# Optimization experiments

Measured on AMD Instinct MI355X. Metric: run time of the kernel, lower is better.

The kernel has to match this reference:

```python
import jax, jax.numpy as jnp
import numpy as np

N_GROUPS = 32
EPS = 1e-5


def group_norm(x, gamma, beta):
    b, c, h, w = x.shape
    xg = x.reshape(b, N_GROUPS, c // N_GROUPS, h, w)
    mean = xg.mean(axis=(2, 3, 4), keepdims=True)
    var = xg.var(axis=(2, 3, 4), keepdims=True)
    xn = ((xg - mean) * jax.lax.rsqrt(var + EPS)).reshape(b, c, h, w)
    return xn * gamma[None, :, None, None] + beta[None, :, None, None]


def conv1x1(x, W, b):
    # x: [b,c,h,w], W: [out,in], b: [out]
    return jnp.einsum('bchw,oc->bohw', x, W) + b[None, :, None, None]


def setup_inputs() -> dict:
    key = jax.random.key(0)
    ks = jax.random.split(key, 6)
    B, C, H, W = 8, 256, 64, 64
    s = 1.0 / np.sqrt(C)
    return {
        'x': jax.random.normal(ks[0], (B, C, H, W), dtype=jnp.float32),
        'norm_gamma': jnp.ones((C,), jnp.float32),
        'norm_beta': jnp.zeros((C,), jnp.float32),
        'Wq': jax.random.normal(ks[1], (C, C), jnp.float32) * s,
        'bq': jnp.zeros((C,), jnp.float32),
        'Wk': jax.random.normal(ks[2], (C, C), jnp.float32) * s,
        'bk': jnp.zeros((C,), jnp.float32),
        'Wv': jax.random.normal(ks[3], (C, C), jnp.float32) * s,
        'bv': jnp.zeros((C,), jnp.float32),
        'Wo': jax.random.normal(ks[4], (C, C), jnp.float32) * s,
        'bo': jnp.zeros((C,), jnp.float32),
    }


def reference(x, norm_gamma, norm_beta, Wq, bq, Wk, bk, Wv, bv, Wo, bo):
    b, c, h, w = x.shape
    hn = group_norm(x, norm_gamma, norm_beta)
    q = conv1x1(hn, Wq, bq).reshape(b, c, h * w)  # [b,c,hw]
    k = conv1x1(hn, Wk, bk).reshape(b, c, h * w)
    v = conv1x1(hn, Wv, bv).reshape(b, c, h * w)
    # scores[b,i,j] = sum_c q[b,c,i] * k[b,c,j]; scale is int(c)*-0.5
    # (faithful to the source, which multiplies by -0.5*c, NOT c**-0.5)
    scores = jnp.einsum('bci,bcj->bij', q, k) * (c * -0.5)
    attn = jax.nn.softmax(scores, axis=2)  # softmax over j (keys)
    # h_[b,c,i] = sum_j v[b,c,j] * attn[b,i,j]
    h_ = jnp.einsum('bcj,bij->bci', v, attn).reshape(b, c, h, w)
    # source applies self.out to the ORIGINAL input x and adds attention output
    return h_ + conv1x1(x, Wo, bo)
```

## Files before the change

### kernel.cpp

```cpp
#include <hip/hip_runtime.h>
#include <hip/hip_bf16.h>


typedef __attribute__((ext_vector_type(8))) short bf16x8;
typedef __attribute__((ext_vector_type(4))) short s16x4;
typedef __attribute__((ext_vector_type(8))) short s16x8;
typedef __attribute__((ext_vector_type(4))) float f32x4;

#define MFMA16(a, b, c) __builtin_amdgcn_mfma_f32_16x16x32_bf16((a), (b), (c), 0, 0, 0)

#define SCALE_Q (-184.66496523378734f)

__device__ __forceinline__ short f2bf(float f) {
  unsigned int u = __builtin_bit_cast(unsigned int, f);
  u = (u + 0x7FFFu + ((u >> 16) & 1u)) >> 16;
  return (short)(unsigned short)u;
}
__device__ __forceinline__ short t2bf(float f) {
  return (short)(__builtin_bit_cast(unsigned int, f) >> 16);
}
__device__ __forceinline__ float bf2f(short h) {
  unsigned int u = ((unsigned int)(unsigned short)h) << 16;
  return __builtin_bit_cast(float, u);
}
__device__ __forceinline__ void async16(void* lds, const void* g) {
  __builtin_amdgcn_global_load_lds(
      (const __attribute__((address_space(1))) unsigned int*)g,
      (__attribute__((address_space(3))) unsigned int*)lds, 16, 0, 0);
}
__device__ __forceinline__ void lgkm_barrier() {
  asm volatile("s_waitcnt lgkmcnt(0)" ::: "memory");
  __builtin_amdgcn_s_barrier();
  __builtin_amdgcn_sched_barrier(0);
}

__global__ void wsplit_k(const float* __restrict__ Wq, const float* __restrict__ Wk,
                         const float* __restrict__ Wv, const float* __restrict__ Wo,
                         short* __restrict__ whi, short* __restrict__ wlo) {
  int idx = blockIdx.x * 256 + threadIdx.x;
  int m = idx >> 16;
  int e = idx & 65535;
  const float* W = (m == 0) ? Wq : (m == 1) ? Wk : (m == 2) ? Wv : Wo;
  float v = W[e];
  short h = f2bf(v);
  whi[idx] = h;
  wlo[idx] = f2bf(v - bf2f(h));
}

__global__ __launch_bounds__(256) void gn_fused_k(
    const float* __restrict__ x, const float* __restrict__ gamma,
    const float* __restrict__ beta, short* __restrict__ hn_hi,
    short* __restrict__ hn_lo) {
  int b = blockIdx.x, g = blockIdx.y, tid = threadIdx.x;
  const float* p = x + ((size_t)(b * 32 + g)) * 32768;
  float s = 0.f, sq = 0.f;
  for (int it = 0; it < 32; ++it) {
    f32x4 v = *(const f32x4*)(p + (size_t)(it * 256 + tid) * 4);
    s += v[0] + v[1] + v[2] + v[3];
    sq += v[0] * v[0] + v[1] * v[1] + v[2] * v[2] + v[3] * v[3];
  }
#pragma unroll
  for (int off = 1; off < 64; off <<= 1) {
    s += __shfl_xor(s, off);
    sq += __shfl_xor(sq, off);
  }
  __shared__ float ls[4], lq[4];
  if ((tid & 63) == 0) { ls[tid >> 6] = s; lq[tid >> 6] = sq; }
  __syncthreads();
  float S = ls[0] + ls[1] + ls[2] + ls[3];
  float Q = lq[0] + lq[1] + lq[2] + lq[3];
  float mean = S * (1.f / 32768.f);
  float rstd = rsqrtf(Q * (1.f / 32768.f) - mean * mean + 1e-5f);
  int c0 = g * 8;
  float ga[8], be[8];
#pragma unroll
  for (int cc = 0; cc < 8; ++cc) {
    ga[cc] = gamma[c0 + cc] * rstd;
    be[cc] = beta[c0 + cc] - mean * ga[cc];
  }
  for (int it = 0; it < 16; ++it) {
    int i = it * 256 + tid;
    s16x8 hv, lv;
#pragma unroll
    for (int cc = 0; cc < 8; ++cc) {
      float xv = p[(size_t)cc * 4096 + i];
      float h = xv * ga[cc] + be[cc];
      short hh = f2bf(h);
      hv[cc] = hh;
      lv[cc] = f2bf(h - bf2f(hh));
    }
    size_t ro = ((size_t)(b * 4096 + i)) * 256 + c0;
    *(s16x8*)(hn_hi + ro) = hv;
    *(s16x8*)(hn_lo + ro) = lv;
  }
}

__global__ __launch_bounds__(256) void proj_qk_k(
    const short* __restrict__ hn_hi, const short* __restrict__ hn_lo,
    const short* __restrict__ whi, const short* __restrict__ wlo,
    const float* __restrict__ bq, const float* __restrict__ bk,
    short* __restrict__ q_hi, short* __restrict__ q_lo,
    short* __restrict__ k_hi, short* __restrict__ k_lo) {
  int tid = threadIdx.x, w = tid >> 6, lane = tid & 63, l4 = lane & 15, g = lane >> 4;
  int iblk = blockIdx.x, y = blockIdx.y, b = blockIdx.z;
  const short* wh = whi + y * 65536;
  const short* wl = wlo + y * 65536;
  const float* bias = y ? bk : bq;
  short* ohi = (y ? k_hi : q_hi) + (size_t)b * 1048576;
  short* olo = (y ? k_lo : q_lo) + (size_t)b * 1048576;
  float scale = y ? 1.0f : SCALE_Q;
  int arow = iblk * 64 + w * 16 + l4;
  const short* ha = hn_hi + ((size_t)(b * 4096 + arow)) * 256 + g * 8;
  const short* la = hn_lo + ((size_t)(b * 4096 + arow)) * 256 + g * 8;
  f32x4 acc[16];
#pragma unroll
  for (int i = 0; i < 16; ++i) acc[i] = (f32x4){0.f, 0.f, 0.f, 0.f};
  for (int ks = 0; ks < 8; ++ks) {
    bf16x8 ah = *(const bf16x8*)(ha + ks * 32);
    bf16x8 al = *(const bf16x8*)(la + ks * 32);
#pragma unroll
    for (int ct = 0; ct < 16; ++ct) {
      bf16x8 bh = *(const bf16x8*)(wh + (ct * 16 + l4) * 256 + ks * 32 + g * 8);
      bf16x8 bl = *(const bf16x8*)(wl + (ct * 16 + l4) * 256 + ks * 32 + g * 8);
      acc[ct] = MFMA16(ah, bh, acc[ct]);
      acc[ct] = MFMA16(al, bh, acc[ct]);
      acc[ct] = MFMA16(ah, bl, acc[ct]);
    }
  }
  int orow = iblk * 64 + w * 16 + g * 4;
#pragma unroll
  for (int ct = 0; ct < 16; ++ct) {
    int c = ct * 16 + l4;
    float bsv = bias[c];
#pragma unroll
    for (int r = 0; r < 4; ++r) {
      float val = (acc[ct][r] + bsv) * scale;
      short h = f2bf(val);
      short lo = f2bf(val - bf2f(h));
      size_t off = ((size_t)(orow + r)) * 256 + c;
      ohi[off] = h;
      olo[off] = lo;
    }
  }
}

__global__ __launch_bounds__(256) void proj_v_k(
    const short* __restrict__ hn_hi, const short* __restrict__ wv_hi,
    const float* __restrict__ bv, short* __restrict__ vout) {
  int tid = threadIdx.x, w = tid >> 6, lane = tid & 63, l4 = lane & 15, g = lane >> 4;
  int jblk = blockIdx.x, cblk = blockIdx.y, b = blockIdx.z;
  int crow = cblk * 64 + w * 16 + l4;
  const short* ap = wv_hi + (size_t)crow * 256 + g * 8;
  f32x4 acc[4];
#pragma unroll
  for (int i = 0; i < 4; ++i) acc[i] = (f32x4){0.f, 0.f, 0.f, 0.f};
  for (int ks = 0; ks < 8; ++ks) {
    bf16x8 a = *(const bf16x8*)(ap + ks * 32);
#pragma unroll
    for (int jt = 0; jt < 4; ++jt) {
      bf16x8 bb = *(const bf16x8*)(hn_hi +
          ((size_t)(b * 4096 + jblk * 64 + jt * 16 + l4)) * 256 + ks * 32 + g * 8);
      acc[jt] = MFMA16(a, bb, acc[jt]);
    }
  }
#pragma unroll
  for (int jt = 0; jt < 4; ++jt) {
#pragma unroll
    for (int r = 0; r < 4; ++r) {
      int c = cblk * 64 + w * 16 + g * 4 + r;
      int j = jblk * 64 + jt * 16 + l4;
      float val = acc[jt][r] + bv[c];
      vout[((size_t)(b * 256 + c)) * 4096 + j] = f2bf(val);
    }
  }
}

__global__ __launch_bounds__(256, 2) void flash3c_k(
    const short* __restrict__ qhi, const short* __restrict__ qlo,
    const short* __restrict__ khi, const short* __restrict__ klo,
    const short* __restrict__ vv, const float* __restrict__ x,
    const short* __restrict__ wo_hi, const float* __restrict__ bo,
    float* __restrict__ out) {
  __shared__ short k_hi_s[2][8192];
  __shared__ short k_lo_s[2][8192];
  __shared__ short p_s[2048];
  __shared__ __attribute__((aligned(16))) float albuf[64];
  __shared__ __attribute__((aligned(16))) float flagbuf[4];
  __shared__ __attribute__((aligned(16))) float lsmbuf[64];

  int tid = threadIdx.x, w = tid >> 6, lane = tid & 63, l4 = lane & 15, g = lane >> 4;
  int b = blockIdx.x, i0 = blockIdx.y * 64;
  size_t boff = (size_t)b * 1048576;
  const short* qh_p = qhi + boff;
  const short* ql_p = qlo + boff;
  const char* kh_g = (const char*)(khi + boff);
  const char* kl_g = (const char*)(klo + boff);
  const short* v_p = vv + boff;

  int qrow = i0 + w * 16 + l4;
  bf16x8 qh[8], ql[8];
#pragma unroll
  for (int ks = 0; ks < 8; ++ks) {
    qh[ks] = *(const bf16x8*)(qh_p + (size_t)qrow * 256 + ks * 32 + g * 8);
    ql[ks] = *(const bf16x8*)(ql_p + (size_t)qrow * 256 + ks * 32 + g * 8);
  }

  f32x4 oac[4][4];
#pragma unroll
  for (int it = 0; it < 4; ++it)
#pragma unroll
    for (int ct = 0; ct < 4; ++ct) oac[it][ct] = (f32x4){0.f, 0.f, 0.f, 0.f};
  float m_cur = -1e30f, lsum = 0.f;

  int ksrc[4];
#pragma unroll
  for (int it = 0; it < 4; ++it) {
    int U = it * 256 + tid;
    int jrow = ((U >> 6) & 1) * 16 + (U & 15);
    ksrc[it] = jrow * 512 + (U >> 7) * 64 + ((U >> 4) & 3) * 16;
  }
  int koff = g * 256 + l4 * 16;
  int pwb = w * 1024 + (g >> 1) * 256 + l4 * 16 + (g & 1) * 8;
  char* khs = (char*)k_hi_s;
  char* kls = (char*)k_lo_s;
  char* ps = (char*)p_s;
  int cbase = w * 64;
  bf16x8 vreg[4];

#pragma unroll
  for (int it = 0; it < 4; ++it) {
    int ldst = w * 1024 + it * 4096;
    async16(khs + ldst, kh_g + ksrc[it]);
    async16(kls + ldst, kl_g + ksrc[it]);
  }

  for (int js = 0; js < 128; ++js) {
    int cur = (js & 1) * 16384;
    __syncthreads();
#pragma unroll
    for (int ct = 0; ct < 4; ++ct)
      vreg[ct] = *(const bf16x8*)(v_p + (size_t)(cbase + ct * 16 + l4) * 4096 +
                                  js * 32 + g * 8);
    if (js < 127) {
      int kgo = (js + 1) * 16384;
      int nxt = ((js + 1) & 1) * 16384;
#pragma unroll
      for (int it = 0; it < 4; ++it) {
        int ldst = nxt + w * 1024 + it * 4096;
        async16(khs + ldst, kh_g + kgo + ksrc[it]);
        async16(kls + ldst, kl_g + kgo + ksrc[it]);
      }
    }

    f32x4 st0 = (f32x4){0.f, 0.f, 0.f, 0.f};
    f32x4 st1 = (f32x4){0.f, 0.f, 0.f, 0.f};
    __builtin_amdgcn_s_setprio(1);
#pragma unroll
    for (int ks = 0; ks < 8; ++ks) {
      bf16x8 kh0 = *(const bf16x8*)(khs + cur + ks * 2048 + koff);
      bf16x8 kh1 = *(const bf16x8*)(khs + cur + ks * 2048 + 1024 + koff);
      bf16x8 kl0 = *(const bf16x8*)(kls + cur + ks * 2048 + koff);
      bf16x8 kl1 = *(const bf16x8*)(kls + cur + ks * 2048 + 1024 + koff);
      st0 = MFMA16(kh0, qh[ks], st0);
      st1 = MFMA16(kh1, qh[ks], st1);
      st0 = MFMA16(kl0, qh[ks], st0);
      st1 = MFMA16(kl1, qh[ks], st1);
      st0 = MFMA16(kh0, ql[ks], st0);
      st1 = MFMA16(kh1, ql[ks], st1);
    }
    __builtin_amdgcn_s_setprio(0);

    float pmax = fmaxf(fmaxf(fmaxf(st0[0], st0[1]), fmaxf(st0[2], st0[3])),
                       fmaxf(fmaxf(st1[0], st1[1]), fmaxf(st1[2], st1[3])));
    pmax = fmaxf(pmax, __shfl_xor(pmax, 16));
    pmax = fmaxf(pmax, __shfl_xor(pmax, 32));
    float alpha = 1.0f;
    bool upd = !__all(pmax <= m_cur + 11.0f);
    if (upd) {
      float m_new = fmaxf(m_cur, pmax);
      alpha = exp2f(m_cur - m_new);
      lsum *= alpha;
      m_cur = m_new;
    }
    f32x4 e0, e1;
#pragma unroll
    for (int r = 0; r < 4; ++r) {
      e0[r] = exp2f(st0[r] - m_cur);
      e1[r] = exp2f(st1[r] - m_cur);
    }
    float lps = e0[0] + e0[1] + e0[2] + e0[3] + e1[0] + e1[1] + e1[2] + e1[3];
    lps += __shfl_xor(lps, 16);
    lps += __shfl_xor(lps, 32);
    lsum += lps;

    s16x4 pw0 = {t2bf(e0[0]), t2bf(e0[1]), t2bf(e0[2]), t2bf(e0[3])};
    s16x4 pw1 = {t2bf(e1[0]), t2bf(e1[1]), t2bf(e1[2]), t2bf(e1[3])};
    *(s16x4*)(ps + pwb) = pw0;
    *(s16x4*)(ps + pwb + 512) = pw1;
    if (lane < 16) albuf[w * 16 + lane] = alpha;
    if (lane == 0) flagbuf[w] = upd ? 1.f : 0.f;

    lgkm_barrier();

    f32x4 fl = *(const f32x4*)(&flagbuf[0]);
    if (fl[0] + fl[1] + fl[2] + fl[3] > 0.f) {
#pragma unroll
      for (int it = 0; it < 4; ++it) {
        f32x4 av = *(const f32x4*)(&albuf[it * 16 + g * 4]);
#pragma unroll
        for (int ct = 0; ct < 4; ++ct)
#pragma unroll
          for (int r = 0; r < 4; ++r) oac[it][ct][r] *= av[r];
      }
    }
    __builtin_amdgcn_s_setprio(1);
#pragma unroll
    for (int it = 0; it < 4; ++it) {
      bf16x8 pf = *(const bf16x8*)(ps + it * 1024 + koff);
#pragma unroll
      for (int ct = 0; ct < 4; ++ct) oac[it][ct] = MFMA16(pf, vreg[ct], oac[it][ct]);
    }
    __builtin_amdgcn_s_setprio(0);
  }

  if (lane < 16) lsmbuf[w * 16 + lane] = lsum;
  __syncthreads();
#pragma unroll
  for (int it = 0; it < 4; ++it) {
    f32x4 lv = *(const f32x4*)(&lsmbuf[it * 16 + g * 4]);
    f32x4 iv = {1.f / lv[0], 1.f / lv[1], 1.f / lv[2], 1.f / lv[3]};
#pragma unroll
    for (int ct = 0; ct < 4; ++ct)
#pragma unroll
      for (int r = 0; r < 4; ++r) oac[it][ct][r] *= iv[r];
  }
  const float* xb = x + (size_t)b * 1048576;
  for (int ks = 0; ks < 8; ++ks) {
    bf16x8 af[4], bfr[4];
#pragma unroll
    for (int it = 0; it < 4; ++it) {
#pragma unroll
      for (int e = 0; e < 8; ++e) {
        float xv = xb[(size_t)(ks * 32 + g * 8 + e) * 4096 + i0 + it * 16 + l4];
        af[it][e] = t2bf(xv);
      }
    }
#pragma unroll
    for (int ct = 0; ct < 4; ++ct)
      bfr[ct] = *(const bf16x8*)(wo_hi + (cbase + ct * 16 + l4) * 256 + ks * 32 + g * 8);
#pragma unroll
    for (int it = 0; it < 4; ++it)
#pragma unroll
      for (int ct = 0; ct < 4; ++ct) oac[it][ct] = MFMA16(af[it], bfr[ct], oac[it][ct]);
  }
  float* ob = out + (size_t)b * 1048576;
#pragma unroll
  for (int ct = 0; ct < 4; ++ct) {
    float bov = bo[cbase + ct * 16 + l4];
#pragma unroll
    for (int it = 0; it < 4; ++it) {
      float* ad = ob + (size_t)(cbase + ct * 16 + l4) * 4096 + i0 + it * 16 + g * 4;
      f32x4 res;
#pragma unroll
      for (int r = 0; r < 4; ++r) res[r] = oac[it][ct][r] + bov;
      *(f32x4*)ad = res;
    }
  }
}

extern "C" void kernel_launch(void* const* d_in, const int* in_sizes, int n_in,
                              void* d_out, int out_size, void* d_ws, size_t ws_size,
                              hipStream_t stream) {
  (void)in_sizes; (void)n_in; (void)out_size; (void)ws_size;
  const float* x = (const float*)d_in[0];
  const float* gamma = (const float*)d_in[1];
  const float* beta = (const float*)d_in[2];
  const float* Wq = (const float*)d_in[3];
  const float* bq = (const float*)d_in[4];
  const float* Wk = (const float*)d_in[5];
  const float* bk = (const float*)d_in[6];
  const float* Wv = (const float*)d_in[7];
  const float* bv = (const float*)d_in[8];
  const float* Wo = (const float*)d_in[9];
  const float* bo = (const float*)d_in[10];
  float* out = (float*)d_out;
  char* ws = (char*)d_ws;

  const size_t MB16 = 16777216;
  short* whi = (short*)(ws + 4096);
  short* wlo = (short*)(ws + 4096 + 524288);
  char* base = ws + 4096 + 2 * 524288;
  short* hnhi = (short*)(base);
  short* hnlo = (short*)(base + MB16);
  short* qhi = (short*)(base + 2 * MB16);
  short* qlo = (short*)(base + 3 * MB16);
  short* khi = (short*)(base + 4 * MB16);
  short* klo = (short*)(base + 5 * MB16);
  short* vvp = (short*)(base + 6 * MB16);

  wsplit_k<<<dim3(1024), dim3(256), 0, stream>>>(Wq, Wk, Wv, Wo, whi, wlo);
  gn_fused_k<<<dim3(8, 32), dim3(256), 0, stream>>>(x, gamma, beta, hnhi, hnlo);
  proj_qk_k<<<dim3(64, 2, 8), dim3(256), 0, stream>>>(hnhi, hnlo, whi, wlo, bq, bk,
                                                      qhi, qlo, khi, klo);
  proj_v_k<<<dim3(64, 4, 8), dim3(256), 0, stream>>>(hnhi, whi + 2 * 65536, bv, vvp);
  flash3c_k<<<dim3(8, 64), dim3(256), 0, stream>>>(qhi, qlo, khi, klo, vvp, x,
                                                   whi + 3 * 65536, bo, out);
}
```

Baseline: 565.8 us.

## Keep softmax probabilities in registers and give each wave all output channels

The PV stage changes from each wave owning 64 output channels for all 64 query rows to each wave owning its own 16 query rows across all 256 channels. The probability tile can then be handed to the MFMA operand through lane shuffles instead of an LDS round trip. This removes the per-iteration LDS writes, the second block barrier, and the alpha/flag exchange buffers, and makes the rescale wave-local. In exchange every wave now loads the full V slab (16 vector loads per iteration, replicated across 4 waves) and holds 16 V registers, which raises global/L2 traffic and register pressure.

```diff
diff --git a/kernel.cpp b/kernel.cpp
--- a/kernel.cpp
+++ b/kernel.cpp
@@ -3,9 +3,9 @@
 
 
 typedef __attribute__((ext_vector_type(8))) short bf16x8;
-typedef __attribute__((ext_vector_type(4))) short s16x4;
 typedef __attribute__((ext_vector_type(8))) short s16x8;
 typedef __attribute__((ext_vector_type(4))) float f32x4;
+typedef __attribute__((ext_vector_type(4))) unsigned u32x4;
 
 #define MFMA16(a, b, c) __builtin_amdgcn_mfma_f32_16x16x32_bf16((a), (b), (c), 0, 0, 0)
 
@@ -19,6 +19,10 @@
 __device__ __forceinline__ short t2bf(float f) {
   return (short)(__builtin_bit_cast(unsigned int, f) >> 16);
 }
+__device__ __forceinline__ unsigned pk2bf(float a, float b) {
+  return (__builtin_bit_cast(unsigned int, b) & 0xFFFF0000u) |
+         (__builtin_bit_cast(unsigned int, a) >> 16);
+}
 __device__ __forceinline__ float bf2f(short h) {
   unsigned int u = ((unsigned int)(unsigned short)h) << 16;
   return __builtin_bit_cast(float, u);
@@ -27,11 +31,6 @@
   __builtin_amdgcn_global_load_lds(
       (const __attribute__((address_space(1))) unsigned int*)g,
       (__attribute__((address_space(3))) unsigned int*)lds, 16, 0, 0);
-}
-__device__ __forceinline__ void lgkm_barrier() {
-  asm volatile("s_waitcnt lgkmcnt(0)" ::: "memory");
-  __builtin_amdgcn_s_barrier();
-  __builtin_amdgcn_sched_barrier(0);
 }
 
 __global__ void wsplit_k(const float* __restrict__ Wq, const float* __restrict__ Wk,
@@ -175,7 +174,7 @@
   }
 }
 
-__global__ __launch_bounds__(256, 2) void flash3c_k(
+__global__ __launch_bounds__(256, 2) void flash6_k(
     const short* __restrict__ qhi, const short* __restrict__ qlo,
     const short* __restrict__ khi, const short* __restrict__ klo,
     const short* __restrict__ vv, const float* __restrict__ x,
@@ -183,10 +182,6 @@
     float* __restrict__ out) {
   __shared__ short k_hi_s[2][8192];
   __shared__ short k_lo_s[2][8192];
-  __shared__ short p_s[2048];
-  __shared__ __attribute__((aligned(16))) float albuf[64];
-  __shared__ __attribute__((aligned(16))) float flagbuf[4];
-  __shared__ __attribute__((aligned(16))) float lsmbuf[64];
 
   int tid = threadIdx.x, w = tid >> 6, lane = tid & 63, l4 = lane & 15, g = lane >> 4;
   int b = blockIdx.x, i0 = blockIdx.y * 64;
@@ -205,11 +200,9 @@
     ql[ks] = *(const bf16x8*)(ql_p + (size_t)qrow * 256 + ks * 32 + g * 8);
   }
 
-  f32x4 oac[4][4];
-#pragma unroll
-  for (int it = 0; it < 4; ++it)
-#pragma unroll
-    for (int ct = 0; ct < 4; ++ct) oac[it][ct] = (f32x4){0.f, 0.f, 0.f, 0.f};
+  f32x4 oac[16];
+#pragma unroll
+  for (int ct = 0; ct < 16; ++ct) oac[ct] = (f32x4){0.f, 0.f, 0.f, 0.f};
   float m_cur = -1e30f, lsum = 0.f;
 
   int ksrc[4];
@@ -220,12 +213,9 @@
     ksrc[it] = jrow * 512 + (U >> 7) * 64 + ((U >> 4) & 3) * 16;
   }
   int koff = g * 256 + l4 * 16;
-  int pwb = w * 1024 + (g >> 1) * 256 + l4 * 16 + (g & 1) * 8;
   char* khs = (char*)k_hi_s;
   char* kls = (char*)k_lo_s;
-  char* ps = (char*)p_s;
-  int cbase = w * 64;
-  bf16x8 vreg[4];
+  bf16x8 vreg[16];
 
 #pragma unroll
   for (int it = 0; it < 4; ++it) {
@@ -234,13 +224,13 @@
     async16(kls + ldst, kl_g + ksrc[it]);
   }
 
+  int srcE = ((g & 1) << 5) + l4;
+  int srcO = srcE + 16;
+  bool gLo = (g < 2);
+
   for (int js = 0; js < 128; ++js) {
     int cur = (js & 1) * 16384;
     __syncthreads();
-#pragma unroll
-    for (int ct = 0; ct < 4; ++ct)
-      vreg[ct] = *(const bf16x8*)(v_p + (size_t)(cbase + ct * 16 + l4) * 4096 +
-                                  js * 32 + g * 8);
     if (js < 127) {
       int kgo = (js + 1) * 16384;
       int nxt = ((js + 1) & 1) * 16384;
@@ -251,6 +241,10 @@
         async16(kls + ldst, kl_g + kgo + ksrc[it]);
       }
     }
+#pragma unroll
+    for (int ct = 0; ct < 16; ++ct)
+      vreg[ct] = *(const bf16x8*)(v_p + (size_t)(ct * 16 + l4) * 4096 +
+                                  js * 32 + g * 8);
 
     f32x4 st0 = (f32x4){0.f, 0.f, 0.f, 0.f};
     f32x4 st1 = (f32x4){0.f, 0.f, 0.f, 0.f};
@@ -274,13 +268,18 @@
                        fmaxf(fmaxf(st1[0], st1[1]), fmaxf(st1[2], st1[3])));
     pmax = fmaxf(pmax, __shfl_xor(pmax, 16));
     pmax = fmaxf(pmax, __shfl_xor(pmax, 32));
-    float alpha = 1.0f;
-    bool upd = !__all(pmax <= m_cur + 11.0f);
-    if (upd) {
+    if (!__all(pmax <= m_cur + 11.0f)) {
       float m_new = fmaxf(m_cur, pmax);
-      alpha = exp2f(m_cur - m_new);
+      float alpha = exp2f(m_cur - m_new);
       lsum *= alpha;
       m_cur = m_new;
+      f32x4 av;
+#pragma unroll
+      for (int r = 0; r < 4; ++r) av[r] = __shfl(alpha, g * 4 + r);
+#pragma unroll
+      for (int ct = 0; ct < 16; ++ct)
+#pragma unroll
+        for (int r = 0; r < 4; ++r) oac[ct][r] *= av[r];
     }
     f32x4 e0, e1;
 #pragma unroll
@@ -293,78 +292,53 @@
     lps += __shfl_xor(lps, 32);
     lsum += lps;
 
-    s16x4 pw0 = {t2bf(e0[0]), t2bf(e0[1]), t2bf(e0[2]), t2bf(e0[3])};
-    s16x4 pw1 = {t2bf(e1[0]), t2bf(e1[1]), t2bf(e1[2]), t2bf(e1[3])};
-    *(s16x4*)(ps + pwb) = pw0;
-    *(s16x4*)(ps + pwb + 512) = pw1;
-    if (lane < 16) albuf[w * 16 + lane] = alpha;
-    if (lane == 0) flagbuf[w] = upd ? 1.f : 0.f;
-
-    lgkm_barrier();
-
-    f32x4 fl = *(const f32x4*)(&flagbuf[0]);
-    if (fl[0] + fl[1] + fl[2] + fl[3] > 0.f) {
-#pragma unroll
-      for (int it = 0; it < 4; ++it) {
-        f32x4 av = *(const f32x4*)(&albuf[it * 16 + g * 4]);
-#pragma unroll
-        for (int ct = 0; ct < 4; ++ct)
-#pragma unroll
-          for (int r = 0; r < 4; ++r) oac[it][ct][r] *= av[r];
-      }
-    }
+    unsigned A0 = pk2bf(e0[0], e0[1]), A1 = pk2bf(e0[2], e0[3]);
+    unsigned B0 = pk2bf(e1[0], e1[1]), B1 = pk2bf(e1[2], e1[3]);
+    unsigned a0E = __shfl((int)A0, srcE), a1E = __shfl((int)A1, srcE);
+    unsigned a0O = __shfl((int)A0, srcO), a1O = __shfl((int)A1, srcO);
+    unsigned b0E = __shfl((int)B0, srcE), b1E = __shfl((int)B1, srcE);
+    unsigned b0O = __shfl((int)B0, srcO), b1O = __shfl((int)B1, srcO);
+    u32x4 pwv = {gLo ? a0E : b0E, gLo ? a1E : b1E,
+                 gLo ? a0O : b0O, gLo ? a1O : b1O};
+    bf16x8 pa = __builtin_bit_cast(bf16x8, pwv);
+
     __builtin_amdgcn_s_setprio(1);
 #pragma unroll
-    for (int it = 0; it < 4; ++it) {
-      bf16x8 pf = *(const bf16x8*)(ps + it * 1024 + koff);
-#pragma unroll
-      for (int ct = 0; ct < 4; ++ct) oac[it][ct] = MFMA16(pf, vreg[ct], oac[it][ct]);
-    }
+    for (int ct = 0; ct < 16; ++ct) oac[ct] = MFMA16(pa, vreg[ct], oac[ct]);
     __builtin_amdgcn_s_setprio(0);
   }
 
-  if (lane < 16) lsmbuf[w * 16 + lane] = lsum;
-  __syncthreads();
-#pragma unroll
-  for (int it = 0; it < 4; ++it) {
-    f32x4 lv = *(const f32x4*)(&lsmbuf[it * 16 + g * 4]);
-    f32x4 iv = {1.f / lv[0], 1.f / lv[1], 1.f / lv[2], 1.f / lv[3]};
-#pragma unroll
-    for (int ct = 0; ct < 4; ++ct)
-#pragma unroll
-      for (int r = 0; r < 4; ++r) oac[it][ct][r] *= iv[r];
-  }
-  const float* xb = x + (size_t)b * 1048576;
+  f32x4 iv;
+#pragma unroll
+  for (int r = 0; r < 4; ++r) iv[r] = 1.f / __shfl(lsum, g * 4 + r);
+#pragma unroll
+  for (int ct = 0; ct < 16; ++ct)
+#pragma unroll
+    for (int r = 0; r < 4; ++r) oac[ct][r] *= iv[r];
+
+  const float* xb = x + boff;
   for (int ks = 0; ks < 8; ++ks) {
-    bf16x8 af[4], bfr[4];
-#pragma unroll
-    for (int it = 0; it < 4; ++it) {
-#pragma unroll
-      for (int e = 0; e < 8; ++e) {
-        float xv = xb[(size_t)(ks * 32 + g * 8 + e) * 4096 + i0 + it * 16 + l4];
-        af[it][e] = t2bf(xv);
-      }
-    }
-#pragma unroll
-    for (int ct = 0; ct < 4; ++ct)
-      bfr[ct] = *(const bf16x8*)(wo_hi + (cbase + ct * 16 + l4) * 256 + ks * 32 + g * 8);
-#pragma unroll
-    for (int it = 0; it < 4; ++it)
-#pragma unroll
-      for (int ct = 0; ct < 4; ++ct) oac[it][ct] = MFMA16(af[it], bfr[ct], oac[it][ct]);
-  }
-  float* ob = out + (size_t)b * 1048576;
-#pragma unroll
-  for (int ct = 0; ct < 4; ++ct) {
-    float bov = bo[cbase + ct * 16 + l4];
-#pragma unroll
-    for (int it = 0; it < 4; ++it) {
-      float* ad = ob + (size_t)(cbase + ct * 16 + l4) * 4096 + i0 + it * 16 + g * 4;
-      f32x4 res;
-#pragma unroll
-      for (int r = 0; r < 4; ++r) res[r] = oac[it][ct][r] + bov;
-      *(f32x4*)ad = res;
-    }
+    bf16x8 af;
+#pragma unroll
+    for (int e = 0; e < 8; ++e) {
+      float xv = xb[(size_t)(ks * 32 + g * 8 + e) * 4096 + i0 + w * 16 + l4];
+      af[e] = t2bf(xv);
+    }
+#pragma unroll
+    for (int ct = 0; ct < 16; ++ct) {
+      bf16x8 bfr = *(const bf16x8*)(wo_hi + (ct * 16 + l4) * 256 + ks * 32 + g * 8);
+      oac[ct] = MFMA16(af, bfr, oac[ct]);
+    }
+  }
+  float* ob = out + boff;
+  int irow = i0 + w * 16 + g * 4;
+#pragma unroll
+  for (int ct = 0; ct < 16; ++ct) {
+    float bov = bo[ct * 16 + l4];
+    f32x4 res;
+#pragma unroll
+    for (int r = 0; r < 4; ++r) res[r] = oac[ct][r] + bov;
+    *(f32x4*)(ob + (size_t)(ct * 16 + l4) * 4096 + irow) = res;
   }
 }
 
@@ -403,6 +377,6 @@
   proj_qk_k<<<dim3(64, 2, 8), dim3(256), 0, stream>>>(hnhi, hnlo, whi, wlo, bq, bk,
                                                       qhi, qlo, khi, klo);
   proj_v_k<<<dim3(64, 4, 8), dim3(256), 0, stream>>>(hnhi, whi + 2 * 65536, bv, vvp);
-  flash3c_k<<<dim3(8, 64), dim3(256), 0, stream>>>(qhi, qlo, khi, klo, vvp, x,
-                                                   whi + 3 * 65536, bo, out);
-}
+  flash6_k<<<dim3(8, 64), dim3(256), 0, stream>>>(qhi, qlo, khi, klo, vvp, x,
+                                                  whi + 3 * 65536, bo, out);
+}
```

New measurement: 929.3 us. +64.2%, slower.
